# Kernel optimization log

Measured on AMD Instinct MI355X. Metric: run time of the kernel, lower is better.

Reference implementation:

```python
import jax, jax.numpy as jnp
import numpy as np

NGRAMS = (1, 2, 3, 4)


def _conv1d(x, W, b):
    # x: [B, S, E], W: [D, E, K], b: [D] -> [B, S-K+1, D] (valid conv, torch Conv1d)
    y = jax.lax.conv_general_dilated(
        x.transpose(0, 2, 1), W, window_strides=(1,), padding='VALID',
        dimension_numbers=('NCH', 'OIH', 'NCH'))
    return y.transpose(0, 2, 1) + b


def setup_inputs() -> dict:
    key = jax.random.key(0)
    ks = jax.random.split(key, 9)
    B, S, E, D = 64, 512, 256, 512
    inp = {'features': jax.random.normal(ks[0], (B, S, E), dtype=jnp.float32)}
    for i, n in enumerate(NGRAMS):
        fan_in = E * n
        inp[f'W{n}'] = jax.random.normal(ks[1 + 2 * i], (D, E, n), dtype=jnp.float32) / np.sqrt(fan_in)
        inp[f'b{n}'] = jax.random.normal(ks[2 + 2 * i], (D,), dtype=jnp.float32) * 0.01
    return inp


def reference(features, W1, b1, W2, b2, W3, b3, W4, b4):
    Ws = (W1, W2, W3, W4)
    bs = (b1, b2, b3, b4)
    # n-gram conv branches: branch g has kernel size NGRAMS[g] = g+1, length S - g
    feats = [_conv1d(features, W, b) for W, b in zip(Ws, bs)]
    B, S, E = features.shape
    flen = E  # faithful to original: features_len = features.shape[-1] (the embed dim)
    out = feats[0]  # unigram features, [B, S, D]
    i = jnp.arange(flen)
    add = jnp.zeros((B, flen, out.shape[-1]), out.dtype)
    # Original nested loops: out[:, i] += sum_{g=1}^{maxn-1} sum_{p=max(0,i-g+1)}^{min(i+1,L_g)-1} feats[g][:, p]
    # Computed here with per-branch prefix sums (exclusive) -> windowed sums.
    for g in range(1, max(NGRAMS)):
        y = feats[g]                      # [B, L, D], L = S - g
        L = y.shape[1]
        P = jnp.concatenate([jnp.zeros_like(y[:, :1]), jnp.cumsum(y, axis=1)], axis=1)  # [B, L+1, D]
        hi = jnp.minimum(i + 1, L)
        lo = jnp.minimum(jnp.maximum(0, i - g + 1), L)
        win = P[:, hi] - P[:, lo]         # [B, flen, D]
        add = add + jnp.where((hi > lo)[None, :, None], win, jnp.zeros_like(win))
    return out.at[:, :flen].add(add)
```

## Files before the change

kernel.cpp:

```cpp
#include <hip/hip_runtime.h>
#include <hip/hip_bf16.h>

#define EDIM 256
#define SDIM 512
#define BDIM 64
#define DDIM 512
#define SPAD 514

#define OFF_XP    0u
#define OFF_GINTB 16842752u
#define OFF_W1B   18415616u
#define OFF_CORR  18677760u
#define OFF_BI    18939904u

#define CVT_BLOCKS  4112
#define WB_BASE     4112
#define CORR_BASE   4624
#define PREP_BLOCKS 8720

typedef __attribute__((ext_vector_type(8))) __bf16 bf16x8;
typedef __attribute__((ext_vector_type(4))) float  f32x4;
typedef __attribute__((ext_vector_type(8))) unsigned short ushort8v;

__device__ __forceinline__ unsigned short f2bf(float f) {
    unsigned int u = __float_as_uint(f);
    u = (u + 0x7fffu + ((u >> 16) & 1u)) >> 16;
    return (unsigned short)u;
}

__global__ __launch_bounds__(256) void prep_all(
    const float* __restrict__ X,
    const float* __restrict__ W1, const float* __restrict__ b1,
    const float* __restrict__ W2, const float* __restrict__ b2,
    const float* __restrict__ W3, const float* __restrict__ b3,
    const float* __restrict__ W4, const float* __restrict__ b4,
    char* __restrict__ wsb)
{
    const int tid = threadIdx.x;

    if (blockIdx.x < CVT_BLOCKS) {
        unsigned short* Xp = (unsigned short*)(wsb + OFF_XP);
        const int i   = blockIdx.x * 256 + tid;
        const int row = i >> 5;
        const int q   = i & 31;
        const int b   = row / SPAD;
        const int j   = row - b * SPAD;
        ushort8v v;
        if (j < 2) {
            v = (ushort8v)0;
        } else {
            const float* src = X + ((size_t)(b * SDIM + j - 2)) * EDIM + q * 8;
            const float4 f0 = *(const float4*)(src);
            const float4 f1 = *(const float4*)(src + 4);
            v[0] = f2bf(f0.x); v[1] = f2bf(f0.y); v[2] = f2bf(f0.z); v[3] = f2bf(f0.w);
            v[4] = f2bf(f1.x); v[5] = f2bf(f1.y); v[6] = f2bf(f1.z); v[7] = f2bf(f1.w);
        }
        *(ushort8v*)(Xp + (size_t)row * EDIM + q * 8) = v;
        return;
    }

    if (blockIdx.x < CORR_BASE) {
        const int d = blockIdx.x - WB_BASE;
        const int e = tid;
        const int de = d * EDIM + e;

        const float w1  = W1[de];
        const float w20 = W2[de * 2 + 0], w21 = W2[de * 2 + 1];
        const float w30 = W3[de * 3 + 0], w31 = W3[de * 3 + 1], w32 = W3[de * 3 + 2];
        const float w40 = W4[de * 4 + 0], w41 = W4[de * 4 + 1], w42 = W4[de * 4 + 2], w43 = W4[de * 4 + 3];

        unsigned short* Gi = (unsigned short*)(wsb + OFF_GINTB) + (size_t)d * 1536;
        Gi[0 * EDIM + e] = f2bf(w40);
        Gi[1 * EDIM + e] = f2bf(w30 + w40 + w41);
        Gi[2 * EDIM + e] = f2bf(w1 + w20 + w30 + w31 + w40 + w41 + w42);
        Gi[3 * EDIM + e] = f2bf(w21 + w31 + w32 + w41 + w42 + w43);
        Gi[4 * EDIM + e] = f2bf(w32 + w42 + w43);
        Gi[5 * EDIM + e] = f2bf(w43);

        ((unsigned short*)(wsb + OFF_W1B))[de] = f2bf(w1);

        if (e == 0)
            ((float*)(wsb + OFF_BI))[d] = b1[d] + b2[d] + 2.0f * b3[d] + 3.0f * b4[d];
        return;
    }

    {
        __shared__ float cls[16];
        const int cb = blockIdx.x - CORR_BASE;
        const int d  = cb >> 3;
        const int bq = (cb & 7) * 8;
        const int e  = tid;

        if (tid < 16) cls[tid] = 0.f;

        const float w31 = W3[(size_t)d * 768 + 3 * e + 1];
        const float w32 = W3[(size_t)d * 768 + 3 * e + 2];
        const float4 w4v = *(const float4*)(W4 + (size_t)d * 1024 + 4 * e);
        const float w41 = w4v.y, w42 = w4v.z, w43 = w4v.w;

        const float c00 = w31 + w41 + w42;
        const float c01 = w32 + w42 + w43;
        const float c02 = w43;
        __syncthreads();

#pragma unroll
        for (int bi = 0; bi < 8; ++bi) {
            const float* xr = X + (size_t)(bq + bi) * (SDIM * EDIM) + e;
            const float x0 = xr[0], x1 = xr[EDIM], x2 = xr[2 * EDIM];
            float a0 = c00 * x0 + c01 * x1 + c02 * x2;
            float a1 = w41 * x0 + w42 * x1 + w43 * x2;
#pragma unroll
            for (int off = 32; off >= 1; off >>= 1) {
                a0 += __shfl_xor(a0, off, 64);
                a1 += __shfl_xor(a1, off, 64);
            }
            if ((tid & 63) == 0) {
                atomicAdd(&cls[bi * 2 + 0], a0);
                atomicAdd(&cls[bi * 2 + 1], a1);
            }
        }
        __syncthreads();

        if (tid < 16) {
            const int s = tid & 1;
            const float bc = s ? b4[d] : (b3[d] + 2.f * b4[d]);
            ((float*)(wsb + OFF_CORR))[(size_t)d * 128 + bq * 2 + tid] = -cls[tid] - bc;
        }
    }
}

#define GLL(src, dst) \
    __builtin_amdgcn_global_load_lds((const __attribute__((address_space(1))) void*)(src), \
                                     (__attribute__((address_space(3))) void*)(dst), 16, 0, 0)

__global__ __launch_bounds__(256) void mega(
    const unsigned short* __restrict__ Xp,
    const char* __restrict__ wsb,
    const float* __restrict__ b1,
    float* __restrict__ out)
{
    __shared__ __align__(16) char smem[32768];
    const int id  = blockIdx.x;
    const int tid = threadIdx.x;

    const bool is_tail = id >= 512;
    const int  idx  = is_tail ? id - 512 : id;
    const int  row0 = (idx & 127) * 128;
    const int  col0 = (idx >> 7) * 128;
    const int  K     = is_tail ? 256 : 1536;
    const int  s_lo  = is_tail ? 256 : 0;
    const int  aoff  = is_tail ? 2 : 0;
    const unsigned short* Gbf = is_tail ? (const unsigned short*)(wsb + OFF_W1B)
                                        : (const unsigned short*)(wsb + OFF_GINTB);
    const float* bias = is_tail ? b1 : (const float*)(wsb + OFF_BI);

    const int w = tid >> 6;
    const int l = tid & 63;

    const int sub = l >> 2;
    const int swz = (((l & 3) ^ ((sub >> 1) & 3)) * 16);

    const int ra0 = row0 + 32 * w + sub;
    const int ra1 = ra0 + 16;
    const int ba0 = ra0 >> 8, sa0 = ra0 & 255;
    const int ba1 = ra1 >> 8, sa1 = ra1 & 255;
    const char* ga0 = (const char*)(Xp + ((size_t)(ba0 * SPAD + s_lo + sa0 + aoff)) * EDIM) + swz;
    const char* ga1 = (const char*)(Xp + ((size_t)(ba1 * SPAD + s_lo + sa1 + aoff)) * EDIM) + swz;
    const char* gb0 = (const char*)(Gbf + (size_t)(col0 + 32 * w + sub) * K) + swz;
    const char* gb1 = (const char*)(Gbf + (size_t)(col0 + 32 * w + 16 + sub) * K) + swz;

    const int oA0 = (32 * w) * 64;
    const int oA1 = (32 * w + 16) * 64;
    const int oB0 = 8192 + (32 * w) * 64;
    const int oB1 = 8192 + (32 * w + 16) * 64;

    char* p0 = smem;
    char* p1 = smem + 16384;

    const int wr  = (w >> 1) * 64;
    const int wc  = (w & 1) * 64;
    const int fm  = l & 15;
    const int rslot = (((l >> 4) ^ ((fm >> 1) & 3)) * 16);
    const int rdA = (wr + fm) * 64 + rslot;
    const int rdB = 8192 + (wc + fm) * 64 + rslot;

    f32x4 acc[4][4] = {};

    auto STAGE = [&](char* buf) {
        GLL(ga0, buf + oA0);
        GLL(ga1, buf + oA1);
        GLL(gb0, buf + oB0);
        GLL(gb1, buf + oB1);
        ga0 += 64; ga1 += 64; gb0 += 64; gb1 += 64;
    };

    auto COMPUTE = [&](const char* buf) {
        bf16x8 af[4], bfr[4];
#pragma unroll
        for (int t = 0; t < 4; ++t) {
            af[t]  = *(const bf16x8*)(buf + rdA + t * 1024);
            bfr[t] = *(const bf16x8*)(buf + rdB + t * 1024);
        }
#pragma unroll
        for (int i = 0; i < 4; ++i)
#pragma unroll
            for (int j = 0; j < 4; ++j)
                acc[i][j] = __builtin_amdgcn_mfma_f32_16x16x32_bf16(af[i], bfr[j], acc[i][j], 0, 0, 0);
    };

    const int nk = K >> 5;

    STAGE(p0);

    for (int kt = 0; kt < nk; ++kt) {
        if (kt < nk - 1) {
            STAGE(p1);
            asm volatile("s_waitcnt vmcnt(4)" ::: "memory");
        } else {
            asm volatile("s_waitcnt vmcnt(0)" ::: "memory");
        }
        __builtin_amdgcn_s_barrier();
        __builtin_amdgcn_s_setprio(1);
        COMPUTE(p0);
        __builtin_amdgcn_s_setprio(0);
        asm volatile("s_waitcnt lgkmcnt(0)" ::: "memory");
        __builtin_amdgcn_s_barrier();
        char* t0 = p0; p0 = p1; p1 = t0;
    }

    const float* corr = (const float*)(wsb + OFF_CORR);
    const int ocol = col0 + wc + fm;
    const int rq   = (l >> 4) * 4;
    float bv[4];
#pragma unroll
    for (int j = 0; j < 4; ++j) bv[j] = bias[ocol + j * 16];

#pragma unroll
    for (int i = 0; i < 4; ++i) {
#pragma unroll
        for (int r = 0; r < 4; ++r) {
            const int rr  = row0 + wr + i * 16 + rq + r;
            const int ssl = rr & 255;
            const int bb  = rr >> 8;
            const int ss  = s_lo + ssl;
            float* op = out + ((size_t)(bb * SDIM + ss)) * DDIM + ocol;
            if (!is_tail && ssl < 2) {
                const float* cp = corr + (size_t)ocol * 128 + bb * 2 + ssl;
#pragma unroll
                for (int j = 0; j < 4; ++j)
                    op[j * 16] = acc[i][j][r] + bv[j] + cp[(size_t)j * 16 * 128];
            } else {
#pragma unroll
                for (int j = 0; j < 4; ++j)
                    op[j * 16] = acc[i][j][r] + bv[j];
            }
        }
    }
}

extern "C" void kernel_launch(void* const* d_in, const int* in_sizes, int n_in,
                              void* d_out, int out_size, void* d_ws, size_t ws_size,
                              hipStream_t stream)
{
    const float* X  = (const float*)d_in[0];
    const float* W1 = (const float*)d_in[1];
    const float* b1 = (const float*)d_in[2];
    const float* W2 = (const float*)d_in[3];
    const float* b2 = (const float*)d_in[4];
    const float* W3 = (const float*)d_in[5];
    const float* b3 = (const float*)d_in[6];
    const float* W4 = (const float*)d_in[7];
    const float* b4 = (const float*)d_in[8];
    float* out = (float*)d_out;
    char*  wsb = (char*)d_ws;

    prep_all<<<dim3(PREP_BLOCKS), dim3(256), 0, stream>>>(X, W1, b1, W2, b2, W3, b3, W4, b4, wsb);

    mega<<<dim3(1024), dim3(256), 0, stream>>>(
        (const unsigned short*)(wsb + OFF_XP), wsb, b1, out);
}
```

Measured before the change: 158.9 us.

## Pre-swizzle B fragments, load B directly to registers, merge tail into head blocks

The weight prep now writes the combined and unigram weight matrices in a fragment-major layout, so each lane can load its MFMA B operand straight from global memory into registers. Only the A tile is staged through LDS, which halves shared memory per block. The tail GEMM (positions 256+) is folded into the same block after the main GEMM, and block IDs are remapped so neighbouring blocks share B columns. The grid drops from 1024 to 512 blocks, which removes launch imbalance between long and short blocks but leaves fewer blocks to hide latency and puts more direct global loads in the inner loop.

```diff
diff --git a/kernel.cpp b/kernel.cpp
--- a/kernel.cpp
+++ b/kernel.cpp
@@ -8,15 +8,15 @@
 #define SPAD 514
 
 #define OFF_XP    0u
-#define OFF_GINTB 16842752u
-#define OFF_W1B   18415616u
+#define OFF_BFI   16842752u
+#define OFF_BFT   18415616u
 #define OFF_CORR  18677760u
 #define OFF_BI    18939904u
 
 #define CVT_BLOCKS  4112
-#define WB_BASE     4112
-#define CORR_BASE   4624
-#define PREP_BLOCKS 8720
+#define BF_BASE     4112
+#define CORR_BASE   4560
+#define PREP_BLOCKS 8656
 
 typedef __attribute__((ext_vector_type(8))) __bf16 bf16x8;
 typedef __attribute__((ext_vector_type(4))) float  f32x4;
@@ -60,27 +60,49 @@
     }
 
     if (blockIdx.x < CORR_BASE) {
-        const int d = blockIdx.x - WB_BASE;
-        const int e = tid;
-        const int de = d * EDIM + e;
-
-        const float w1  = W1[de];
-        const float w20 = W2[de * 2 + 0], w21 = W2[de * 2 + 1];
-        const float w30 = W3[de * 3 + 0], w31 = W3[de * 3 + 1], w32 = W3[de * 3 + 2];
-        const float w40 = W4[de * 4 + 0], w41 = W4[de * 4 + 1], w42 = W4[de * 4 + 2], w43 = W4[de * 4 + 3];
-
-        unsigned short* Gi = (unsigned short*)(wsb + OFF_GINTB) + (size_t)d * 1536;
-        Gi[0 * EDIM + e] = f2bf(w40);
-        Gi[1 * EDIM + e] = f2bf(w30 + w40 + w41);
-        Gi[2 * EDIM + e] = f2bf(w1 + w20 + w30 + w31 + w40 + w41 + w42);
-        Gi[3 * EDIM + e] = f2bf(w21 + w31 + w32 + w41 + w42 + w43);
-        Gi[4 * EDIM + e] = f2bf(w32 + w42 + w43);
-        Gi[5 * EDIM + e] = f2bf(w43);
-
-        ((unsigned short*)(wsb + OFF_W1B))[de] = f2bf(w1);
-
-        if (e == 0)
-            ((float*)(wsb + OFF_BI))[d] = b1[d] + b2[d] + 2.0f * b3[d] + 3.0f * b4[d];
+        const int p  = blockIdx.x - BF_BASE;
+        const int t  = tid >> 6;
+        const int l  = tid & 63;
+        const int fm = l & 15;
+        const int hi = l >> 4;
+        if (p < 384) {
+            const int kt = p % 48;
+            const int h  = (p / 48) & 1;
+            const int c  = p / 96;
+            const int d  = c * 128 + h * 64 + t * 16 + fm;
+            const int shift = kt >> 3;
+            const int e0 = (kt & 7) * 32 + hi * 8;
+            ushort8v v;
+#pragma unroll
+            for (int j = 0; j < 8; ++j) {
+                const int e  = e0 + j;
+                const int de = d * 256 + e;
+                float g;
+                if      (shift == 0) g = W4[de*4+0];
+                else if (shift == 1) g = W3[de*3+0] + W4[de*4+0] + W4[de*4+1];
+                else if (shift == 2) g = W1[de] + W2[de*2+0] + W3[de*3+0] + W3[de*3+1]
+                                       + W4[de*4+0] + W4[de*4+1] + W4[de*4+2];
+                else if (shift == 3) g = W2[de*2+1] + W3[de*3+1] + W3[de*3+2]
+                                       + W4[de*4+1] + W4[de*4+2] + W4[de*4+3];
+                else if (shift == 4) g = W3[de*3+2] + W4[de*4+2] + W4[de*4+3];
+                else                 g = W4[de*4+3];
+                v[j] = f2bf(g);
+            }
+            *(ushort8v*)(wsb + OFF_BFI + (size_t)((((c*2+h)*48 + kt)*4 + t)*1024 + l*16)) = v;
+            if (kt == 0 && hi == 0)
+                ((float*)(wsb + OFF_BI))[d] = b1[d] + b2[d] + 2.0f*b3[d] + 3.0f*b4[d];
+        } else {
+            const int q  = p - 384;
+            const int kt = q % 8;
+            const int h  = (q / 8) & 1;
+            const int c  = q / 16;
+            const int d  = c * 128 + h * 64 + t * 16 + fm;
+            const int k0 = kt * 32 + hi * 8;
+            ushort8v v;
+#pragma unroll
+            for (int j = 0; j < 8; ++j) v[j] = f2bf(W1[d * 256 + k0 + j]);
+            *(ushort8v*)(wsb + OFF_BFT + (size_t)((((c*2+h)*8 + kt)*4 + t)*1024 + l*16)) = v;
+        }
         return;
     }
 
@@ -139,68 +161,54 @@
     const float* __restrict__ b1,
     float* __restrict__ out)
 {
-    __shared__ __align__(16) char smem[32768];
-    const int id  = blockIdx.x;
+    __shared__ __align__(16) char smem[16384];
+    const int id0 = blockIdx.x;
+    const int id  = (id0 & 7) * 64 + (id0 >> 3);
+    const int strip = id & 127;
+    const int c     = id >> 7;
+    const int col0  = c * 128;
     const int tid = threadIdx.x;
-
-    const bool is_tail = id >= 512;
-    const int  idx  = is_tail ? id - 512 : id;
-    const int  row0 = (idx & 127) * 128;
-    const int  col0 = (idx >> 7) * 128;
-    const int  K     = is_tail ? 256 : 1536;
-    const int  s_lo  = is_tail ? 256 : 0;
-    const int  aoff  = is_tail ? 2 : 0;
-    const unsigned short* Gbf = is_tail ? (const unsigned short*)(wsb + OFF_W1B)
-                                        : (const unsigned short*)(wsb + OFF_GINTB);
-    const float* bias = is_tail ? b1 : (const float*)(wsb + OFF_BI);
-
-    const int w = tid >> 6;
-    const int l = tid & 63;
+    const int w = tid >> 6, l = tid & 63;
 
     const int sub = l >> 2;
     const int swz = (((l & 3) ^ ((sub >> 1) & 3)) * 16);
-
-    const int ra0 = row0 + 32 * w + sub;
+    const int ra0 = strip * 128 + 32 * w + sub;
     const int ra1 = ra0 + 16;
     const int ba0 = ra0 >> 8, sa0 = ra0 & 255;
     const int ba1 = ra1 >> 8, sa1 = ra1 & 255;
-    const char* ga0 = (const char*)(Xp + ((size_t)(ba0 * SPAD + s_lo + sa0 + aoff)) * EDIM) + swz;
-    const char* ga1 = (const char*)(Xp + ((size_t)(ba1 * SPAD + s_lo + sa1 + aoff)) * EDIM) + swz;
-    const char* gb0 = (const char*)(Gbf + (size_t)(col0 + 32 * w + sub) * K) + swz;
-    const char* gb1 = (const char*)(Gbf + (size_t)(col0 + 32 * w + 16 + sub) * K) + swz;
 
     const int oA0 = (32 * w) * 64;
     const int oA1 = (32 * w + 16) * 64;
-    const int oB0 = 8192 + (32 * w) * 64;
-    const int oB1 = 8192 + (32 * w + 16) * 64;
-
-    char* p0 = smem;
-    char* p1 = smem + 16384;
-
-    const int wr  = (w >> 1) * 64;
-    const int wc  = (w & 1) * 64;
-    const int fm  = l & 15;
+    char* pc = smem;
+    char* pn = smem + 8192;
+
+    const int wr = (w >> 1) * 64;
+    const int h  = w & 1;
+    const int wc = h * 64;
+    const int fm = l & 15;
     const int rslot = (((l >> 4) ^ ((fm >> 1) & 3)) * 16);
-    const int rdA = (wr + fm) * 64 + rslot;
-    const int rdB = 8192 + (wc + fm) * 64 + rslot;
-
-    f32x4 acc[4][4] = {};
-
+
+    const char* bfi = wsb + OFF_BFI + (size_t)(c * 2 + h) * (48 * 4096) + l * 16;
+    const char* bft = wsb + OFF_BFT + (size_t)(c * 2 + h) * (8 * 4096) + l * 16;
+
+    f32x4 acc[4][4];
+    const char *a0, *a1;
+
+    auto LOADB = [&](bf16x8 (&dst)[4], const char* base, int kt) {
+#pragma unroll
+        for (int t = 0; t < 4; ++t)
+            dst[t] = *(const bf16x8*)(base + (size_t)kt * 4096 + t * 1024);
+    };
     auto STAGE = [&](char* buf) {
-        GLL(ga0, buf + oA0);
-        GLL(ga1, buf + oA1);
-        GLL(gb0, buf + oB0);
-        GLL(gb1, buf + oB1);
-        ga0 += 64; ga1 += 64; gb0 += 64; gb1 += 64;
-    };
-
-    auto COMPUTE = [&](const char* buf) {
-        bf16x8 af[4], bfr[4];
-#pragma unroll
-        for (int t = 0; t < 4; ++t) {
-            af[t]  = *(const bf16x8*)(buf + rdA + t * 1024);
-            bfr[t] = *(const bf16x8*)(buf + rdB + t * 1024);
-        }
+        GLL(a0, buf + oA0);
+        GLL(a1, buf + oA1);
+        a0 += 64; a1 += 64;
+    };
+    auto COMP = [&](const char* buf, const bf16x8 (&bfr)[4]) {
+        bf16x8 af[4];
+#pragma unroll
+        for (int t = 0; t < 4; ++t)
+            af[t] = *(const bf16x8*)(buf + (wr + t * 16 + fm) * 64 + rslot);
 #pragma unroll
         for (int i = 0; i < 4; ++i)
 #pragma unroll
@@ -208,54 +216,84 @@
                 acc[i][j] = __builtin_amdgcn_mfma_f32_16x16x32_bf16(af[i], bfr[j], acc[i][j], 0, 0, 0);
     };
 
-    const int nk = K >> 5;
-
-    STAGE(p0);
-
-    for (int kt = 0; kt < nk; ++kt) {
-        if (kt < nk - 1) {
-            STAGE(p1);
-            asm volatile("s_waitcnt vmcnt(4)" ::: "memory");
-        } else {
-            asm volatile("s_waitcnt vmcnt(0)" ::: "memory");
-        }
-        __builtin_amdgcn_s_barrier();
-        __builtin_amdgcn_s_setprio(1);
-        COMPUTE(p0);
-        __builtin_amdgcn_s_setprio(0);
-        asm volatile("s_waitcnt lgkmcnt(0)" ::: "memory");
-        __builtin_amdgcn_s_barrier();
-        char* t0 = p0; p0 = p1; p1 = t0;
-    }
-
-    const float* corr = (const float*)(wsb + OFF_CORR);
-    const int ocol = col0 + wc + fm;
-    const int rq   = (l >> 4) * 4;
-    float bv[4];
-#pragma unroll
-    for (int j = 0; j < 4; ++j) bv[j] = bias[ocol + j * 16];
-
-#pragma unroll
-    for (int i = 0; i < 4; ++i) {
-#pragma unroll
-        for (int r = 0; r < 4; ++r) {
-            const int rr  = row0 + wr + i * 16 + rq + r;
-            const int ssl = rr & 255;
-            const int bb  = rr >> 8;
-            const int ss  = s_lo + ssl;
-            float* op = out + ((size_t)(bb * SDIM + ss)) * DDIM + ocol;
-            if (!is_tail && ssl < 2) {
-                const float* cp = corr + (size_t)ocol * 128 + bb * 2 + ssl;
-#pragma unroll
-                for (int j = 0; j < 4; ++j)
-                    op[j * 16] = acc[i][j][r] + bv[j] + cp[(size_t)j * 16 * 128];
+    auto GEMM = [&](const char* bbase, int nk) {
+        bf16x8 bA[4], bB[4];
+        LOADB(bA, bbase, 0);
+        STAGE(pc);
+#pragma unroll 1
+        for (int kt = 0; kt < nk; kt += 2) {
+            STAGE(pn);
+            LOADB(bB, bbase, kt + 1);
+            asm volatile("s_waitcnt vmcnt(6)" ::: "memory");
+            __builtin_amdgcn_s_barrier();
+            __builtin_amdgcn_s_setprio(1);
+            COMP(pc, bA);
+            __builtin_amdgcn_s_setprio(0);
+            asm volatile("s_waitcnt lgkmcnt(0)" ::: "memory");
+            __builtin_amdgcn_s_barrier();
+            if (kt + 2 < nk) {
+                STAGE(pc);
+                LOADB(bA, bbase, kt + 2);
+                asm volatile("s_waitcnt vmcnt(6)" ::: "memory");
             } else {
-#pragma unroll
-                for (int j = 0; j < 4; ++j)
-                    op[j * 16] = acc[i][j][r] + bv[j];
-            }
-        }
-    }
+                asm volatile("s_waitcnt vmcnt(0)" ::: "memory");
+            }
+            __builtin_amdgcn_s_barrier();
+            __builtin_amdgcn_s_setprio(1);
+            COMP(pn, bB);
+            __builtin_amdgcn_s_setprio(0);
+            asm volatile("s_waitcnt lgkmcnt(0)" ::: "memory");
+            __builtin_amdgcn_s_barrier();
+        }
+    };
+
+    auto EPI = [&](int s_base, bool with_corr) {
+        const float* bias = with_corr ? (const float*)(wsb + OFF_BI) : b1;
+        const float* corr = (const float*)(wsb + OFF_CORR);
+        const int ocol = col0 + wc + fm;
+        const int rq   = (l >> 4) * 4;
+        float bv[4];
+#pragma unroll
+        for (int j = 0; j < 4; ++j) bv[j] = bias[ocol + j * 16];
+#pragma unroll
+        for (int i = 0; i < 4; ++i) {
+#pragma unroll
+            for (int r = 0; r < 4; ++r) {
+                const int rr  = strip * 128 + wr + i * 16 + rq + r;
+                const int ssl = rr & 255;
+                const int bb  = rr >> 8;
+                float* op = out + ((size_t)(bb * SDIM + s_base + ssl)) * DDIM + ocol;
+                if (with_corr && ssl < 2) {
+                    const float* cp = corr + (size_t)ocol * 128 + bb * 2 + ssl;
+#pragma unroll
+                    for (int j = 0; j < 4; ++j)
+                        op[j * 16] = acc[i][j][r] + bv[j] + cp[(size_t)j * 16 * 128];
+                } else {
+#pragma unroll
+                    for (int j = 0; j < 4; ++j)
+                        op[j * 16] = acc[i][j][r] + bv[j];
+                }
+            }
+        }
+    };
+
+#pragma unroll
+    for (int i = 0; i < 4; ++i)
+#pragma unroll
+        for (int j = 0; j < 4; ++j) acc[i][j] = (f32x4){0.f, 0.f, 0.f, 0.f};
+    a0 = (const char*)(Xp + (size_t)(ba0 * SPAD + sa0) * EDIM) + swz;
+    a1 = (const char*)(Xp + (size_t)(ba1 * SPAD + sa1) * EDIM) + swz;
+    GEMM(bfi, 48);
+    EPI(0, true);
+
+#pragma unroll
+    for (int i = 0; i < 4; ++i)
+#pragma unroll
+        for (int j = 0; j < 4; ++j) acc[i][j] = (f32x4){0.f, 0.f, 0.f, 0.f};
+    a0 = (const char*)(Xp + (size_t)(ba0 * SPAD + 258 + sa0) * EDIM) + swz;
+    a1 = (const char*)(Xp + (size_t)(ba1 * SPAD + 258 + sa1) * EDIM) + swz;
+    GEMM(bft, 8);
+    EPI(256, false);
 }
 
 extern "C" void kernel_launch(void* const* d_in, const int* in_sizes, int n_in,
@@ -276,6 +314,6 @@
 
     prep_all<<<dim3(PREP_BLOCKS), dim3(256), 0, stream>>>(X, W1, b1, W2, b2, W3, b3, W4, b4, wsb);
 
-    mega<<<dim3(1024), dim3(256), 0, stream>>>(
+    mega<<<dim3(512), dim3(256), 0, stream>>>(
         (const unsigned short*)(wsb + OFF_XP), wsb, b1, out);
 }
```

Measured after the change: 169.5 us. 1.07x slower.
